# Kernel optimization log

Hardware: AMD Instinct MI355X
Metric: run time of the kernel (lower is better)

The kernel has to match this reference:

```python
import jax, jax.numpy as jnp
import numpy as np

D_MODEL = 1024
NUM_HEADS = 16
D_K = D_MODEL // NUM_HEADS


def setup_inputs() -> dict:
    key = jax.random.key(0)
    ks = jax.random.split(key, 12)
    B, S, D = 4, 1024, D_MODEL
    s = 1.0 / np.sqrt(D)
    inp = {
        "query": jax.random.normal(ks[0], (B, S, D), jnp.float32),
        "key": jax.random.normal(ks[1], (B, S, D), jnp.float32),
        "value": jax.random.normal(ks[2], (B, S, D), jnp.float32),
        "mask": jnp.ones((B, S, S), dtype=bool),
        # Linear params, torch convention: W has shape [out, in], y = x @ W.T + b
        "Wq": jax.random.normal(ks[3], (D, D), jnp.float32) * s,
        "bq": jax.random.normal(ks[4], (D,), jnp.float32) * s,
        "Wk": jax.random.normal(ks[5], (D, D), jnp.float32) * s,
        "bk": jax.random.normal(ks[6], (D,), jnp.float32) * s,
        "Wv": jax.random.normal(ks[7], (D, D), jnp.float32) * s,
        "bv": jax.random.normal(ks[8], (D,), jnp.float32) * s,
        "Wo": jax.random.normal(ks[9], (D, D), jnp.float32) * s,
        "bo": jax.random.normal(ks[10], (D,), jnp.float32) * s,
    }
    return inp


def reference(query, key, value, mask, Wq, bq, Wk, bk, Wv, bv, Wo, bo):
    B, S, D = query.shape
    H, dk = NUM_HEADS, D_K

    def split_heads(x):  # [B,S,D] -> [B,H,S,dk]
        return x.reshape(B, S, H, dk).transpose(0, 2, 1, 3)

    Q = split_heads(query @ Wq.T + bq)
    K = split_heads(key @ Wk.T + bk)
    V = split_heads(value @ Wv.T + bv)

    scores = jnp.einsum("bhqd,bhkd->bhqk", Q, K) / jnp.sqrt(jnp.float32(dk))
    # mask: [B,S,S] -> [B,1,S,S]; 0/False positions masked to -inf
    scores = jnp.where(mask[:, None, :, :], scores, -jnp.inf)
    attn_weights = jax.nn.softmax(scores, axis=-1)  # [B,H,S,S]
    out = jnp.einsum("bhqk,bhkd->bhqd", attn_weights, V)
    out = out.transpose(0, 2, 1, 3).reshape(B, S, D)
    out = out @ Wo.T + bo  # dropout is identity (eval / p=0)
    return out, attn_weights
```

## Files before the change

### kernel.cpp

```cpp
#include <hip/hip_runtime.h>
#include <hip/hip_bf16.h>

#define SS 1024
#define DD 1024
#define HH 16
#define DK 64
#define MM 4096

typedef __attribute__((ext_vector_type(4))) float f32x4;
typedef __attribute__((ext_vector_type(8))) short bf16x8;
typedef __attribute__((ext_vector_type(4))) _Float16 f16x4;

typedef __attribute__((address_space(3))) unsigned int lds_u32;
typedef __attribute__((address_space(1))) const unsigned int glb_u32;

__device__ __forceinline__ short f2bf(float x) {
  unsigned u = __builtin_bit_cast(unsigned, x);
  u += 0x7FFFu + ((u >> 16) & 1u);
  return (short)(u >> 16);
}

__global__ __launch_bounds__(256) void convert6(
    const float* __restrict__ q, const float* __restrict__ k, const float* __restrict__ v,
    const float* __restrict__ wq, const float* __restrict__ wk, const float* __restrict__ wv,
    short* __restrict__ dst)
{
  const int u = blockIdx.x * 256 + threadIdx.x;
  const float* s;
  short* d;
  if (u < 1572864) {
    const int which = u >> 19;
    const size_t loc = (size_t)(u & 524287) * 8;
    s = (which == 0 ? q : which == 1 ? k : v) + loc;
    d = dst + (size_t)which * 4194304 + loc;
  } else {
    const int v2 = u - 1572864;
    const int which = v2 >> 17;
    const size_t loc = (size_t)(v2 & 131071) * 8;
    s = (which == 0 ? wq : which == 1 ? wk : wv) + loc;
    d = dst + 12582912 + (size_t)which * 1048576 + loc;
  }
  float4 a = *(const float4*)s;
  float4 c = *(const float4*)(s + 4);
  short r[8];
  r[0] = f2bf(a.x); r[1] = f2bf(a.y); r[2] = f2bf(a.z); r[3] = f2bf(a.w);
  r[4] = f2bf(c.x); r[5] = f2bf(c.y); r[6] = f2bf(c.z); r[7] = f2bf(c.w);
  *(uint4*)d = *(const uint4*)r;
}

__global__ __launch_bounds__(256) void convert1(const float* __restrict__ w,
                                                short* __restrict__ d)
{
  const int u = blockIdx.x * 256 + threadIdx.x;
  const size_t loc = (size_t)u * 8;
  float4 a = *(const float4*)(w + loc);
  float4 c = *(const float4*)(w + loc + 4);
  short r[8];
  r[0] = f2bf(a.x); r[1] = f2bf(a.y); r[2] = f2bf(a.z); r[3] = f2bf(a.w);
  r[4] = f2bf(c.x); r[5] = f2bf(c.y); r[6] = f2bf(c.z); r[7] = f2bf(c.w);
  *(uint4*)(d + loc) = *(const uint4*)r;
}

template <int EPI>
__global__ __launch_bounds__(256) void gemm128(
    const short* __restrict__ Abase, const short* __restrict__ Bbase,
    const float* __restrict__ b0, const float* __restrict__ b1, const float* __restrict__ b2,
    short* __restrict__ Obf, float* __restrict__ Of)
{
  const int z = blockIdx.z;
  const short* A = Abase + (size_t)z * 4194304;
  const short* B = Bbase + (size_t)z * 1048576;
  const float* bias = z == 0 ? b0 : (z == 1 ? b1 : b2);
  short* O = Obf + (size_t)z * 4194304;

  __shared__ short As[8192];
  __shared__ short Bs[8192];

  const int t = threadIdx.x, lane = t & 63, w = t >> 6;
  const int m0 = blockIdx.y * 128, n0 = blockIdx.x * 128;
  const int wm = (w >> 1) * 64, wn = (w & 1) * 64;

  f32x4 acc[4][4];
#pragma unroll
  for (int a = 0; a < 4; ++a)
#pragma unroll
    for (int b = 0; b < 4; ++b) acc[a][b] = (f32x4){0.f, 0.f, 0.f, 0.f};

  const int rb = lane >> 3;
  const int cj = (lane & 7) ^ rb;

  for (int kt = 0; kt < 16; ++kt) {
    const int k0 = kt * 64;
    __syncthreads();
#pragma unroll
    for (int i = 0; i < 4; ++i) {
      const int seg = w * 4 + i;
      const int r = seg * 8 + rb;
      __builtin_amdgcn_global_load_lds(
          (glb_u32*)(A + (size_t)(m0 + r) * DD + k0 + cj * 8),
          (lds_u32*)((char*)As + seg * 1024), 16, 0, 0);
      __builtin_amdgcn_global_load_lds(
          (glb_u32*)(B + (size_t)(n0 + r) * DD + k0 + cj * 8),
          (lds_u32*)((char*)Bs + seg * 1024), 16, 0, 0);
    }
    asm volatile("s_waitcnt vmcnt(0)" ::: "memory");
    __syncthreads();

    bf16x8 af[4][2], bg[4][2];
#pragma unroll
    for (int f = 0; f < 4; ++f)
#pragma unroll
      for (int kk = 0; kk < 2; ++kk) {
        const int c = kk * 4 + (lane >> 4);
        const int ra = wm + f * 16 + (lane & 15);
        af[f][kk] = *(const bf16x8*)((const char*)As + ra * 128 + (((c ^ (ra & 7))) << 4));
        const int rbn = wn + f * 16 + (lane & 15);
        bg[f][kk] = *(const bf16x8*)((const char*)Bs + rbn * 128 + (((c ^ (rbn & 7))) << 4));
      }
#pragma unroll
    for (int fm = 0; fm < 4; ++fm)
#pragma unroll
      for (int fn = 0; fn < 4; ++fn) {
        acc[fm][fn] = __builtin_amdgcn_mfma_f32_16x16x32_bf16(af[fm][0], bg[fn][0], acc[fm][fn], 0, 0, 0);
        acc[fm][fn] = __builtin_amdgcn_mfma_f32_16x16x32_bf16(af[fm][1], bg[fn][1], acc[fm][fn], 0, 0, 0);
      }
  }

#pragma unroll
  for (int fn = 0; fn < 4; ++fn) {
    const int col = n0 + wn + fn * 16 + (lane & 15);
    const float bvv = bias[col];
    if (EPI == 0) {
      const int h = col >> 6, d = col & 63;
#pragma unroll
      for (int fm = 0; fm < 4; ++fm)
#pragma unroll
        for (int j = 0; j < 4; ++j) {
          const int rowm = m0 + wm + fm * 16 + (lane >> 4) * 4 + j;
          const int b = rowm >> 10, s = rowm & 1023;
          const float val = acc[fm][fn][j] + bvv;
          short outv;
          if (z == 2) {
            _Float16 hv = (_Float16)val;
            outv = __builtin_bit_cast(short, hv);
          } else {
            outv = f2bf(val);
          }
          O[((size_t)(b * HH + h) * SS + s) * DK + d] = outv;
        }
    } else {
#pragma unroll
      for (int fm = 0; fm < 4; ++fm)
#pragma unroll
        for (int j = 0; j < 4; ++j) {
          const int rowm = m0 + wm + fm * 16 + (lane >> 4) * 4 + j;
          Of[(size_t)rowm * DD + col] = acc[fm][fn][j] + bvv;
        }
    }
  }
}

__global__ __launch_bounds__(256) void transposeV(
    const short* __restrict__ Vh, short* __restrict__ Vtg)
{
  const int kt = blockIdx.x;
  const int bh = blockIdx.y;
  const short* Vb = Vh + (size_t)bh * SS * DK;
  short* Ob = Vtg + (size_t)bh * DK * SS;
  const int t = threadIdx.x;

  __shared__ short Vs[64 * 72];

  {
    const int r = t >> 2, c = (t & 3) * 16;
    const short* src = Vb + (size_t)(kt * 64 + r) * DK + c;
    *(uint4*)&Vs[r * 72 + c]     = *(const uint4*)src;
    *(uint4*)&Vs[r * 72 + c + 8] = *(const uint4*)(src + 8);
  }
  __syncthreads();
  {
    const int d = t >> 2, kc = (t & 3) * 16;
    short vals[16];
#pragma unroll
    for (int jj = 0; jj < 16; ++jj) vals[jj] = Vs[(kc + jj) * 72 + d];
    short* dst = Ob + (size_t)d * SS + kt * 64 + kc;
    *(uint4*)dst       = *(const uint4*)&vals[0];
    *(uint4*)(dst + 8) = *(const uint4*)&vals[8];
  }
}

__global__ __launch_bounds__(256, 3) void attn_q16(
    const short* __restrict__ Qh, const short* __restrict__ Kh, const short* __restrict__ Vtg,
    float* __restrict__ attn, short* __restrict__ Oh)
{
  const int wg = blockIdx.x;
  const int bh = (wg & 7) * 8 + ((wg >> 3) & 7);
  const int qb = wg >> 6;
  const int b = bh >> 4, h = bh & 15;
  const short* Qb = Qh + ((size_t)bh * SS + qb * 16) * DK;
  const short* Kb = Kh + (size_t)bh * SS * DK;
  const short* Vtb = Vtg + (size_t)bh * DK * SS;
  const int t = threadIdx.x, lane = t & 63, wid = t >> 6;
  const int q15 = lane & 15, g = lane >> 4;

  __shared__ __align__(16) char smem[51712];
  short* Pt   = (short*)smem;
  short* Ks   = (short*)(smem + 33024);
  short* Vt   = (short*)(smem + 42240);
  float* lsum = (float*)(smem + 51456);
  short* Qs   = (short*)smem;
  float* obuf = (float*)(smem + 33024);

  if (t < 128) {
    const int r = t >> 3, c = (t & 7) * 8;
    *(uint4*)&Qs[r * 72 + c] = *(const uint4*)(Qb + (size_t)r * DK + c);
  }
  __syncthreads();
  bf16x8 aq0 = *(const bf16x8*)&Qs[q15 * 72 + g * 8];
  bf16x8 aq1 = *(const bf16x8*)&Qs[q15 * 72 + 32 + g * 8];
  asm volatile("s_waitcnt lgkmcnt(0)" ::: "memory");
  __builtin_amdgcn_sched_barrier(0);

  const int kr = t >> 2, kc = (t & 3) * 16;
  const int vr2 = t >> 2, vc2 = (t & 3) * 16;
  const int hsw = ((vr2 >> 3) & 7) << 3;
  uint4 kreg0 = *(const uint4*)(Kb + (size_t)kr * DK + kc);
  uint4 kreg1 = *(const uint4*)(Kb + (size_t)kr * DK + kc + 8);
  uint4 vreg0 = *(const uint4*)(Vtb + (size_t)vr2 * SS + vc2);
  uint4 vreg1 = *(const uint4*)(Vtb + (size_t)vr2 * SS + vc2 + 8);

  f32x4 accO[4];
#pragma unroll
  for (int fd = 0; fd < 4; ++fd) accO[fd] = (f32x4){0.f, 0.f, 0.f, 0.f};
  float lacc = 0.f;

  for (int kt = 0; kt < 16; ++kt) {
    __syncthreads();
    *(uint4*)&Ks[kr * 72 + kc]     = kreg0;
    *(uint4*)&Ks[kr * 72 + kc + 8] = kreg1;
    *(uint4*)&Vt[vr2 * 72 + (vc2 ^ hsw)]       = vreg0;
    *(uint4*)&Vt[vr2 * 72 + ((vc2 + 8) ^ hsw)] = vreg1;
    if (kt < 15) {
      const short* Kn = Kb + (size_t)(kt + 1) * 64 * DK;
      const short* Vn = Vtb + (size_t)(kt + 1) * 64;
      kreg0 = *(const uint4*)(Kn + (size_t)kr * DK + kc);
      kreg1 = *(const uint4*)(Kn + (size_t)kr * DK + kc + 8);
      vreg0 = *(const uint4*)(Vn + (size_t)vr2 * SS + vc2);
      vreg1 = *(const uint4*)(Vn + (size_t)vr2 * SS + vc2 + 8);
    }
    __syncthreads();

    f32x4 zz;
    {
      const short* kp = &Ks[(wid * 16 + q15) * 72];
      bf16x8 ak0 = *(const bf16x8*)(kp + g * 8);
      bf16x8 ak1 = *(const bf16x8*)(kp + 32 + g * 8);
      f32x4 z0 = (f32x4){0.f, 0.f, 0.f, 0.f};
      z0 = __builtin_amdgcn_mfma_f32_16x16x32_bf16(ak0, aq0, z0, 0, 0, 0);
      z0 = __builtin_amdgcn_mfma_f32_16x16x32_bf16(ak1, aq1, z0, 0, 0, 0);
      zz = z0;
    }

    f16x4 pf;
#pragma unroll
    for (int j = 0; j < 4; ++j) {
      const float pe = __expf(zz[j] * 0.125f);
      lacc += pe;
      pf[j] = (_Float16)pe;
    }
    {
      const int pcb = (kt * 64 + wid * 16 + g * 4) ^ (((q15 >> 3) & 1) << 4);
      *(f16x4*)&Pt[q15 * 1032 + pcb] = pf;
    }

#pragma unroll
    for (int fd = 0; fd < 4; ++fd) {
      const int d = fd * 16 + q15;
      const int kcol = (wid * 16 + g * 4) ^ (((d >> 3) & 7) << 3);
      f16x4 vf = *(const f16x4*)&Vt[d * 72 + kcol];
      accO[fd] = __builtin_amdgcn_mfma_f32_16x16x16f16(pf, vf, accO[fd], 0, 0, 0);
    }
  }

  {
    float s = lacc;
    s += __shfl_xor(s, 16);
    s += __shfl_xor(s, 32);
    if (lane < 16) lsum[wid * 16 + lane] = s;
  }
  __syncthreads();

  if (wid > 0) {
    float* ob = obuf + (wid - 1) * 1088;
#pragma unroll
    for (int fd = 0; fd < 4; ++fd)
#pragma unroll
      for (int j = 0; j < 4; ++j)
        ob[(g * 4 + j) * 68 + fd * 16 + q15] = accO[fd][j];
  }
  __syncthreads();

  if (wid == 0) {
#pragma unroll
    for (int j = 0; j < 4; ++j) {
      const int q = g * 4 + j;
      const float rl = __builtin_amdgcn_rcpf(lsum[q] + lsum[16 + q] + lsum[32 + q] + lsum[48 + q]);
      const int qs = qb * 16 + q;
#pragma unroll
      for (int fd = 0; fd < 4; ++fd) {
        const int d = fd * 16 + q15;
        const float o = (accO[fd][j] + obuf[q * 68 + d] + obuf[1088 + q * 68 + d]
                         + obuf[2176 + q * 68 + d]) * rl;
        Oh[((size_t)b * SS + qs) * DD + h * DK + d] = f2bf(o);
      }
    }
  }

  float* attnB = attn + ((size_t)bh * SS + qb * 16) * SS;
  for (int i = 0; i < 16; ++i) {
    const float rl = __builtin_amdgcn_rcpf(lsum[i] + lsum[16 + i] + lsum[32 + i] + lsum[48 + i]);
    const int pc = (t * 4) ^ (((i >> 3) & 1) << 4);
    const uint2 rd = *(const uint2*)&Pt[i * 1032 + pc];
    float4 o;
    o.x = (float)__builtin_bit_cast(_Float16, (unsigned short)(rd.x & 0xffff)) * rl;
    o.y = (float)__builtin_bit_cast(_Float16, (unsigned short)(rd.x >> 16)) * rl;
    o.z = (float)__builtin_bit_cast(_Float16, (unsigned short)(rd.y & 0xffff)) * rl;
    o.w = (float)__builtin_bit_cast(_Float16, (unsigned short)(rd.y >> 16)) * rl;
    *(float4*)&attnB[(size_t)i * SS + t * 4] = o;
  }
}

extern "C" void kernel_launch(void* const* d_in, const int* in_sizes, int n_in,
                              void* d_out, int out_size, void* d_ws, size_t ws_size,
                              hipStream_t stream) {
  const float* q  = (const float*)d_in[0];
  const float* k  = (const float*)d_in[1];
  const float* v  = (const float*)d_in[2];
  const float* Wq = (const float*)d_in[4];  const float* bq = (const float*)d_in[5];
  const float* Wk = (const float*)d_in[6];  const float* bk = (const float*)d_in[7];
  const float* Wv = (const float*)d_in[8];  const float* bv = (const float*)d_in[9];
  const float* Wo = (const float*)d_in[10]; const float* bo = (const float*)d_in[11];

  float* out  = (float*)d_out;
  float* attn = out + (size_t)MM * DD;

  short* Qh = (short*)d_ws;
  short* Kh = Qh + (size_t)MM * DD;
  short* Vh = Kh + (size_t)MM * DD;
  short* Ohb = Vh + (size_t)MM * DD;

  short* S = (short*)attn;
  short* Wbf = S + 12582912;

  short* Vtg = (short*)out;

  convert6<<<7680, 256, 0, stream>>>(q, k, v, Wq, Wk, Wv, S);
  gemm128<0><<<dim3(8, 32, 3), 256, 0, stream>>>(S, Wbf, bq, bk, bv, Qh, nullptr);
  transposeV<<<dim3(16, 64), 256, 0, stream>>>(Vh, Vtg);
  attn_q16<<<4096, 256, 0, stream>>>(Qh, Kh, Vtg, attn, Ohb);
  convert1<<<512, 256, 0, stream>>>(Wo, Qh);
  gemm128<1><<<dim3(8, 32, 1), 256, 0, stream>>>(Ohb, Qh, bo, bo, bo, nullptr, out);
}
```

Measured before the change: 183.7 us.

## Load K/V tiles directly to LDS via global_load_lds with XOR swizzle

Replaces the register-staged K and V tile loads (global to VGPR prefetch, then ds_write) with direct global-to-LDS loads via global_load_lds, using an XOR-swizzled unpadded 64-wide layout. LDS reads are updated to match the new swizzle, and the shared buffer shrinks. This drops the register prefetch, so the loads are no longer overlapped with the previous tile's compute, and a vmcnt(0) wait now blocks before each tile is used.

```diff
diff --git a/kernel.cpp b/kernel.cpp
--- a/kernel.cpp
+++ b/kernel.cpp
@@ -203,11 +203,11 @@
   const int t = threadIdx.x, lane = t & 63, wid = t >> 6;
   const int q15 = lane & 15, g = lane >> 4;
 
-  __shared__ __align__(16) char smem[51712];
+  __shared__ __align__(16) char smem[49664];
   short* Pt   = (short*)smem;
   short* Ks   = (short*)(smem + 33024);
-  short* Vt   = (short*)(smem + 42240);
-  float* lsum = (float*)(smem + 51456);
+  short* Vt   = (short*)(smem + 41216);
+  float* lsum = (float*)(smem + 49408);
   short* Qs   = (short*)smem;
   float* obuf = (float*)(smem + 33024);
 
@@ -221,13 +221,8 @@
   asm volatile("s_waitcnt lgkmcnt(0)" ::: "memory");
   __builtin_amdgcn_sched_barrier(0);
 
-  const int kr = t >> 2, kc = (t & 3) * 16;
-  const int vr2 = t >> 2, vc2 = (t & 3) * 16;
-  const int hsw = ((vr2 >> 3) & 7) << 3;
-  uint4 kreg0 = *(const uint4*)(Kb + (size_t)kr * DK + kc);
-  uint4 kreg1 = *(const uint4*)(Kb + (size_t)kr * DK + kc + 8);
-  uint4 vreg0 = *(const uint4*)(Vtb + (size_t)vr2 * SS + vc2);
-  uint4 vreg1 = *(const uint4*)(Vtb + (size_t)vr2 * SS + vc2 + 8);
+  const int srow = lane >> 3;
+  const int schunk = (lane & 7) ^ srow;
 
   f32x4 accO[4];
 #pragma unroll
@@ -236,25 +231,32 @@
 
   for (int kt = 0; kt < 16; ++kt) {
     __syncthreads();
-    *(uint4*)&Ks[kr * 72 + kc]     = kreg0;
-    *(uint4*)&Ks[kr * 72 + kc + 8] = kreg1;
-    *(uint4*)&Vt[vr2 * 72 + (vc2 ^ hsw)]       = vreg0;
-    *(uint4*)&Vt[vr2 * 72 + ((vc2 + 8) ^ hsw)] = vreg1;
-    if (kt < 15) {
-      const short* Kn = Kb + (size_t)(kt + 1) * 64 * DK;
-      const short* Vn = Vtb + (size_t)(kt + 1) * 64;
-      kreg0 = *(const uint4*)(Kn + (size_t)kr * DK + kc);
-      kreg1 = *(const uint4*)(Kn + (size_t)kr * DK + kc + 8);
-      vreg0 = *(const uint4*)(Vn + (size_t)vr2 * SS + vc2);
-      vreg1 = *(const uint4*)(Vn + (size_t)vr2 * SS + vc2 + 8);
-    }
+    {
+      const int rK0 = wid * 16 + srow;
+      const short* Ksrc0 = Kb + (size_t)(kt * 64 + rK0) * DK + schunk * 8;
+      __builtin_amdgcn_global_load_lds((glb_u32*)Ksrc0,
+          (lds_u32*)((char*)Ks + wid * 2048), 16, 0, 0);
+      const short* Ksrc1 = Kb + (size_t)(kt * 64 + rK0 + 8) * DK + schunk * 8;
+      __builtin_amdgcn_global_load_lds((glb_u32*)Ksrc1,
+          (lds_u32*)((char*)Ks + wid * 2048 + 1024), 16, 0, 0);
+      const int rV0 = wid * 16 + srow;
+      const short* Vsrc0 = Vtb + (size_t)rV0 * SS + kt * 64 + schunk * 8;
+      __builtin_amdgcn_global_load_lds((glb_u32*)Vsrc0,
+          (lds_u32*)((char*)Vt + wid * 2048), 16, 0, 0);
+      const short* Vsrc1 = Vtb + (size_t)(rV0 + 8) * SS + kt * 64 + schunk * 8;
+      __builtin_amdgcn_global_load_lds((glb_u32*)Vsrc1,
+          (lds_u32*)((char*)Vt + wid * 2048 + 1024), 16, 0, 0);
+    }
+    asm volatile("s_waitcnt vmcnt(0)" ::: "memory");
     __syncthreads();
 
     f32x4 zz;
     {
-      const short* kp = &Ks[(wid * 16 + q15) * 72];
-      bf16x8 ak0 = *(const bf16x8*)(kp + g * 8);
-      bf16x8 ak1 = *(const bf16x8*)(kp + 32 + g * 8);
+      const int row = wid * 16 + q15;
+      const int key = q15 & 7;
+      const short* kp = &Ks[row * 64];
+      bf16x8 ak0 = *(const bf16x8*)(kp + ((g ^ key) * 8));
+      bf16x8 ak1 = *(const bf16x8*)(kp + (((g + 4) ^ key) * 8));
       f32x4 z0 = (f32x4){0.f, 0.f, 0.f, 0.f};
       z0 = __builtin_amdgcn_mfma_f32_16x16x32_bf16(ak0, aq0, z0, 0, 0, 0);
       z0 = __builtin_amdgcn_mfma_f32_16x16x32_bf16(ak1, aq1, z0, 0, 0, 0);
@@ -276,8 +278,8 @@
 #pragma unroll
     for (int fd = 0; fd < 4; ++fd) {
       const int d = fd * 16 + q15;
-      const int kcol = (wid * 16 + g * 4) ^ (((d >> 3) & 7) << 3);
-      f16x4 vf = *(const f16x4*)&Vt[d * 72 + kcol];
+      const int vchunk = (wid * 2 + (g >> 1)) ^ (d & 7);
+      f16x4 vf = *(const f16x4*)&Vt[d * 64 + vchunk * 8 + (g & 1) * 4];
       accO[fd] = __builtin_amdgcn_mfma_f32_16x16x16f16(pf, vf, accO[fd], 0, 0, 0);
     }
   }
```

Measured after the change: 213.1 us. +16.0%, slower.
